# Optimization experiments

Measured on AMD Instinct MI355X. Metric: run time of the kernel, lower is better.

## Reference

```python
import jax, jax.numpy as jnp
import numpy as np

EMBED_DIM = 1024
NUM_HEADS = 16
HEAD_DIM = EMBED_DIM // NUM_HEADS


def setup_inputs() -> dict:
    key = jax.random.key(0)
    ks = jax.random.split(key, 11)
    B, S, D = 2, 2048, EMBED_DIM
    s = 1.0 / np.sqrt(D)
    inp = {
        "query": jax.random.normal(ks[0], (B, S, D), jnp.float32),
        "key": jax.random.normal(ks[1], (B, S, D), jnp.float32),
        "value": jax.random.normal(ks[2], (B, S, D), jnp.float32),
        # torch Linear weights: [out, in]
        "Wq": jax.random.normal(ks[3], (D, D), jnp.float32) * s,
        "bq": jnp.zeros((D,), jnp.float32),
        "Wk": jax.random.normal(ks[4], (D, D), jnp.float32) * s,
        "bk": jnp.zeros((D,), jnp.float32),
        "Wv": jax.random.normal(ks[5], (D, D), jnp.float32) * s,
        "bv": jnp.zeros((D,), jnp.float32),
        "Wo": jax.random.normal(ks[6], (D, D), jnp.float32) * s,
        "bo": jnp.zeros((D,), jnp.float32),
    }
    return inp


def reference(query, key, value, Wq, bq, Wk, bk, Wv, bv, Wo, bo):
    B, Q, D = query.shape
    K = key.shape[1]
    H, Hd = NUM_HEADS, HEAD_DIM
    # NOTE: source divides by scaling = head_dim**-0.5, i.e. multiplies by sqrt(head_dim)
    scaling = float(Hd) ** (-0.5)

    q = (query @ Wq.T + bq).reshape(B, Q, H, Hd).transpose(0, 2, 1, 3)  # [B,H,Q,Hd]
    k = (key @ Wk.T + bk).reshape(B, K, H, Hd).transpose(0, 2, 1, 3)    # [B,H,K,Hd]
    v = (value @ Wv.T + bv).reshape(B, K, H, Hd).transpose(0, 2, 1, 3)  # [B,H,K,Hd]

    scores = jnp.einsum("bhqd,bhkd->bhqk", q, k) / scaling
    attn = jax.nn.softmax(scores, axis=-1)  # dropout=0 (eval)
    out = jnp.einsum("bhqk,bhkd->bhqd", attn, v)
    out = out.transpose(0, 2, 1, 3).reshape(B, Q, D)
    return out @ Wo.T + bo
```

## Files before the change

kernel.cpp:

```cpp
#include <hip/hip_runtime.h>
#include <type_traits>
#include <utility>

#define B_ 2
#define S_ 2048
#define D_ 1024
#define H_ 16
#define HD_ 64
#define KDIM 1024

typedef __attribute__((ext_vector_type(8))) short    s16x8;
typedef __attribute__((ext_vector_type(8))) _Float16 h16x8;
typedef __attribute__((ext_vector_type(4))) float    f32x4;
typedef __attribute__((ext_vector_type(4))) int      i32x4;
typedef __attribute__((ext_vector_type(2))) int      i32x2;

template <typename T, typename = void> struct mfma_takes : std::false_type {};
template <typename T>
struct mfma_takes<T, std::void_t<decltype(__builtin_amdgcn_mfma_f32_16x16x32_f16(
    std::declval<T>(), std::declval<T>(), std::declval<f32x4>(), 0, 0, 0))>>
    : std::true_type {};
using frag8 = std::conditional_t<mfma_takes<h16x8>::value, h16x8, s16x8>;

__device__ __forceinline__ f32x4 mfma_f16(frag8 a, frag8 b, f32x4 c) {
  return __builtin_amdgcn_mfma_f32_16x16x32_f16(a, b, c, 0, 0, 0);
}

__device__ __forceinline__ short f2h(float f) {
  _Float16 h = (_Float16)f;
  short s; __builtin_memcpy(&s, &h, 2);
  return s;
}
__device__ __forceinline__ int pk2h(float a, float b) {
  auto p = __builtin_amdgcn_cvt_pkrtz(a, b);
  int r; __builtin_memcpy(&r, &p, 4); return r;
}
__device__ __forceinline__ frag8 ld_frag(const short* p) {
  return __builtin_bit_cast(frag8, *(const i32x4*)p);
}
__device__ __forceinline__ float fast_exp2(float x) {
  return __builtin_amdgcn_exp2f(x);
}

typedef __attribute__((address_space(1))) const void gvoid;
typedef __attribute__((address_space(3))) void lvoid;
__device__ __forceinline__ void async_copy16(const void* g, void* l) {
  __builtin_amdgcn_global_load_lds((gvoid*)g, (lvoid*)l, 16, 0, 0);
}

#define RAW_BARRIER() asm volatile("s_barrier" ::: "memory")
#define WAITCNT_VM(n) asm volatile("s_waitcnt vmcnt(" #n ")" ::: "memory")

__global__ __launch_bounds__(256)
void conv_all(const float* __restrict__ q, const float* __restrict__ k,
              const float* __restrict__ v, const float* __restrict__ Wq,
              const float* __restrict__ Wk, const float* __restrict__ Wv,
              const float* __restrict__ Wo,
              short* __restrict__ qh, short* __restrict__ kh,
              short* __restrict__ vh, short* __restrict__ wq,
              short* __restrict__ wk, short* __restrict__ wv,
              short* __restrict__ wo) {
  const int blk = blockIdx.x;
  const float* src; short* dst; int base;
  if (blk < 2048)      { src = q;  dst = qh; base = blk; }
  else if (blk < 4096) { src = k;  dst = kh; base = blk - 2048; }
  else if (blk < 6144) { src = v;  dst = vh; base = blk - 4096; }
  else if (blk < 6656) { src = Wq; dst = wq; base = blk - 6144; }
  else if (blk < 7168) { src = Wk; dst = wk; base = blk - 6656; }
  else if (blk < 7680) { src = Wv; dst = wv; base = blk - 7168; }
  else                 { src = Wo; dst = wo; base = blk - 7680; }
  const int i = base * 2048 + threadIdx.x * 8;
  float4 a0 = *(const float4*)(src + i);
  float4 a1 = *(const float4*)(src + i + 4);
  short h[8] = { f2h(a0.x), f2h(a0.y), f2h(a0.z), f2h(a0.w),
                 f2h(a1.x), f2h(a1.y), f2h(a1.z), f2h(a1.w) };
  i32x4 ph; __builtin_memcpy(&ph, h, 16);
  *(i32x4*)(dst + i) = ph;
}

__global__ __launch_bounds__(256, 3)
void gemm_qkv(const short* __restrict__ qh, const short* __restrict__ kh,
              const short* __restrict__ vh, const short* __restrict__ wq,
              const short* __restrict__ wk, const short* __restrict__ wv,
              const float* __restrict__ bq, const float* __restrict__ bk,
              const float* __restrict__ bv, short* __restrict__ Qf,
              short* __restrict__ Kf, short* __restrict__ Vt, float QS) {
  __shared__ short As[3 * 4096];
  __shared__ short Bs[3 * 4096];

  const int blk = blockIdx.x;
  const int xcd = blk & 7, i = blk >> 3;
  const int p = (i >> 3) * 8 + xcd;
  const int bn = i & 7;
  const int z = p >> 5, bm = p & 31;
  const short* Ap = z == 0 ? qh : z == 1 ? kh : vh;
  const short* Wp = z == 0 ? wq : z == 1 ? wk : wv;
  const float* bias = z == 0 ? bq : z == 1 ? bk : bv;
  short* Out = z == 0 ? Qf : z == 1 ? Kf : Vt;
  const float scale = z == 0 ? QS : 1.0f;
  const int omode = z == 2 ? 2 : 1;

  const int t = threadIdx.x, wave = t >> 6, lane = t & 63;
  const int laneN = lane & 15, quad = lane >> 4;
  const int wm = wave & 1, wn = wave >> 1;

  f32x4 acc[4][4];
#pragma unroll
  for (int i2 = 0; i2 < 4; ++i2)
#pragma unroll
    for (int j = 0; j < 4; ++j)
#pragma unroll
      for (int r = 0; r < 4; ++r) acc[i2][j][r] = 0.f;

  auto stage = [&](int buf, int kk) {
#pragma unroll
    for (int j = 0; j < 2; ++j) {
      const int chunk = j * 256 + t;
      const int row = chunk >> 2;
      const int gg = (chunk & 3) ^ ((row >> 1) & 3);
      async_copy16(Ap + (size_t)(bm * 128 + row) * KDIM + kk + gg * 8,
                   As + buf * 4096 + chunk * 8);
      async_copy16(Wp + (size_t)(bn * 128 + row) * KDIM + kk + gg * 8,
                   Bs + buf * 4096 + chunk * 8);
    }
  };

  stage(0, 0);
  stage(1, 32);
  int buf = 0;
  for (int kk = 0; kk < KDIM; kk += 32) {
    if (kk + 64 < KDIM) {
      int nb = buf + 2; if (nb >= 3) nb -= 3;
      stage(nb, kk + 64);
      WAITCNT_VM(8);
    } else if (kk + 32 < KDIM) {
      WAITCNT_VM(4);
    } else {
      WAITCNT_VM(0);
    }
    RAW_BARRIER();

    frag8 aF[4], bF[4];
#pragma unroll
    for (int mi = 0; mi < 4; ++mi) {
      const int row = wm * 64 + mi * 16 + laneN;
      aF[mi] = ld_frag(As + buf * 4096 + row * 32 +
                       ((quad ^ ((row >> 1) & 3)) * 8));
    }
#pragma unroll
    for (int ni = 0; ni < 4; ++ni) {
      const int row = wn * 64 + ni * 16 + laneN;
      bF[ni] = ld_frag(Bs + buf * 4096 + row * 32 +
                       ((quad ^ ((row >> 1) & 3)) * 8));
    }
#pragma unroll
    for (int mi = 0; mi < 4; ++mi)
#pragma unroll
      for (int ni = 0; ni < 4; ++ni)
        acc[mi][ni] = mfma_f16(aF[mi], bF[ni], acc[mi][ni]);
    RAW_BARRIER();
    buf = buf + 1 == 3 ? 0 : buf + 1;
  }

#pragma unroll
  for (int mi = 0; mi < 4; ++mi)
#pragma unroll
    for (int ni = 0; ni < 4; ++ni) {
      const int colg = bn * 128 + wn * 64 + ni * 16 + laneN;
      const float bb = bias[colg];
      if (omode == 2) {
        const int rowg0 = bm * 128 + wm * 64 + mi * 16 + quad * 4;
        const int b = rowg0 >> 11, s0 = rowg0 & 2047;
        const int h = colg >> 6, hd = colg & 63;
        short pk[4];
#pragma unroll
        for (int r = 0; r < 4; ++r) pk[r] = f2h(acc[mi][ni][r] + bb);
        i32x2 w; __builtin_memcpy(&w, pk, 8);
        *(i32x2*)(Vt + (((size_t)(b * H_ + h)) * HD_ + hd) * S_ + s0) = w;
      } else {
#pragma unroll
        for (int r = 0; r < 4; ++r) {
          const int rowg = bm * 128 + wm * 64 + mi * 16 + quad * 4 + r;
          const int b = rowg >> 11, s = rowg & 2047;
          const int h = colg >> 6, hd = colg & 63;
          Out[(((size_t)(b * H_ + h)) * S_ + s) * HD_ + hd] =
              f2h((acc[mi][ni][r] + bb) * scale);
        }
      }
    }
}

__global__ __launch_bounds__(256, 3)
void gemm_out(const short* __restrict__ Ap, const short* __restrict__ Wp,
              const float* __restrict__ bias, float* __restrict__ Out) {
  __shared__ short As[3 * 4096];
  __shared__ short Bs[3 * 2048];
  const int blk = blockIdx.x;
  const int xcd = blk & 7, i = blk >> 3;
  const int bm = (i >> 4) * 8 + xcd;
  const int bn = i & 15;

  const int t = threadIdx.x, wave = t >> 6, lane = t & 63;
  const int laneN = lane & 15, quad = lane >> 4;
  const int wm = wave & 1, wn = wave >> 1;

  f32x4 acc[4][2];
#pragma unroll
  for (int i2 = 0; i2 < 4; ++i2)
#pragma unroll
    for (int j = 0; j < 2; ++j)
#pragma unroll
      for (int r = 0; r < 4; ++r) acc[i2][j][r] = 0.f;

  auto stage = [&](int buf, int kk) {
#pragma unroll
    for (int j = 0; j < 2; ++j) {
      const int chunk = j * 256 + t;
      const int row = chunk >> 2;
      const int gg = (chunk & 3) ^ ((row >> 1) & 3);
      async_copy16(Ap + (size_t)(bm * 128 + row) * KDIM + kk + gg * 8,
                   As + buf * 4096 + chunk * 8);
    }
    {
      const int chunk = t;
      const int row = chunk >> 2;
      const int gg = (chunk & 3) ^ ((row >> 1) & 3);
      async_copy16(Wp + (size_t)(bn * 64 + row) * KDIM + kk + gg * 8,
                   Bs + buf * 2048 + chunk * 8);
    }
  };

  stage(0, 0);
  stage(1, 32);
  int buf = 0;
  for (int kk = 0; kk < KDIM; kk += 32) {
    if (kk + 64 < KDIM) {
      int nb = buf + 2; if (nb >= 3) nb -= 3;
      stage(nb, kk + 64);
      WAITCNT_VM(6);
    } else if (kk + 32 < KDIM) {
      WAITCNT_VM(3);
    } else {
      WAITCNT_VM(0);
    }
    RAW_BARRIER();

    frag8 aF[4], bF[2];
#pragma unroll
    for (int mi = 0; mi < 4; ++mi) {
      const int row = wm * 64 + mi * 16 + laneN;
      aF[mi] = ld_frag(As + buf * 4096 + row * 32 +
                       ((quad ^ ((row >> 1) & 3)) * 8));
    }
#pragma unroll
    for (int ni = 0; ni < 2; ++ni) {
      const int row = wn * 32 + ni * 16 + laneN;
      bF[ni] = ld_frag(Bs + buf * 2048 + row * 32 +
                       ((quad ^ ((row >> 1) & 3)) * 8));
    }
#pragma unroll
    for (int mi = 0; mi < 4; ++mi)
#pragma unroll
      for (int ni = 0; ni < 2; ++ni)
        acc[mi][ni] = mfma_f16(aF[mi], bF[ni], acc[mi][ni]);
    RAW_BARRIER();
    buf = buf + 1 == 3 ? 0 : buf + 1;
  }

#pragma unroll
  for (int mi = 0; mi < 4; ++mi)
#pragma unroll
    for (int ni = 0; ni < 2; ++ni) {
      const int colg = bn * 64 + wn * 32 + ni * 16 + laneN;
      const float bb = bias[colg];
#pragma unroll
      for (int r = 0; r < 4; ++r) {
        const int rowg = bm * 128 + wm * 64 + mi * 16 + quad * 4 + r;
        Out[(size_t)rowg * 1024 + colg] = acc[mi][ni][r] + bb;
      }
    }
}

__global__ __launch_bounds__(512, 2)
void attn(const short* __restrict__ Qf, const short* __restrict__ Kf,
          const short* __restrict__ Vt_, short* __restrict__ Ow) {
  __shared__ short Ks[2 * 4096];
  __shared__ short Vts[2 * 4096];
  __shared__ short Ps[8][16 * 72];

  const int blk = blockIdx.x;
  const int xcd = blk & 7, local = blk >> 3;
  const int pair = xcd * 4 + (local >> 4);
  const int h = pair & 15, b = pair >> 4, qt = local & 15;
  const size_t head = ((size_t)b * H_ + h) * (size_t)S_ * HD_;

  const int t = threadIdx.x;
  const int wave = t >> 6, lane = t & 63;
  const int laneN = lane & 15, quad = lane >> 4;

  frag8 qf[2];
  {
    const size_t row = (size_t)qt * 128 + wave * 16 + laneN;
#pragma unroll
    for (int half = 0; half < 2; ++half)
      qf[half] = ld_frag(Qf + head + row * HD_ + half * 32 + quad * 8);
  }

  f32x4 o[4];
  float m_r = -1e30f, l_r = 0.f;
#pragma unroll
  for (int i = 0; i < 4; ++i)
#pragma unroll
    for (int j = 0; j < 4; ++j) o[i][j] = 0.f;

  auto stage = [&](int buf, int kt) {
    const int chunk = t;
    const int row = chunk >> 3;
    const int g = (chunk & 7) ^ (row & 7);
    const int ldsoff = buf * 4096 + chunk * 8;
    async_copy16(Kf + head + (size_t)(kt * 64 + row) * HD_ + g * 8, Ks + ldsoff);
    async_copy16(Vt_ + head + (size_t)row * S_ + kt * 64 + g * 8, Vts + ldsoff);
  };

  stage(0, 0);
  int buf = 0;
  for (int kt = 0; kt < 32; ++kt, buf ^= 1) {
    if (kt + 1 < 32) {
      stage(buf ^ 1, kt + 1);
      WAITCNT_VM(2);
    } else {
      WAITCNT_VM(0);
    }
    RAW_BARRIER();

    frag8 vf[4][2];
#pragma unroll
    for (int dt = 0; dt < 4; ++dt) {
      const int row = dt * 16 + laneN;
#pragma unroll
      for (int half = 0; half < 2; ++half)
        vf[dt][half] = ld_frag(Vts + buf * 4096 + row * 64 +
                               (((half * 4 + quad) ^ (row & 7)) * 8));
    }

    f32x4 s[4];
#pragma unroll
    for (int nt = 0; nt < 4; ++nt) {
      const int row = nt * 16 + laneN;
      const int o0 = buf * 4096 + row * 64 + ((quad ^ (row & 7)) * 8);
      const int o1 = buf * 4096 + row * 64 + (((quad + 4) ^ (row & 7)) * 8);
      frag8 k0 = ld_frag(Ks + o0), k1 = ld_frag(Ks + o1);
      f32x4 acc;
#pragma unroll
      for (int j = 0; j < 4; ++j) acc[j] = 0.f;
      acc = mfma_f16(k0, qf[0], acc);
      acc = mfma_f16(k1, qf[1], acc);
      s[nt] = acc;
    }

    {
      float mx = -1e30f;
#pragma unroll
      for (int nt = 0; nt < 4; ++nt)
#pragma unroll
        for (int r = 0; r < 4; ++r) mx = fmaxf(mx, s[nt][r]);
      mx = fmaxf(mx, __shfl_xor(mx, 16));
      mx = fmaxf(mx, __shfl_xor(mx, 32));
      const float mold = m_r;
      const float mn = fmaxf(mold, mx);
      float rs = 0.f;
#pragma unroll
      for (int nt = 0; nt < 4; ++nt)
#pragma unroll
        for (int r = 0; r < 4; ++r) {
          const float p = fast_exp2(s[nt][r] - mn);
          s[nt][r] = p; rs += p;
        }
      rs += __shfl_xor(rs, 16);
      rs += __shfl_xor(rs, 32);
      if (__any(mn > mold)) {
        const float al = fast_exp2(mold - mn);
        m_r = mn;
        l_r = l_r * al + rs;
#pragma unroll
        for (int dt = 0; dt < 4; ++dt)
#pragma unroll
          for (int r = 0; r < 4; ++r) o[dt][r] *= al;
      } else {
        l_r += rs;
      }
    }

#pragma unroll
    for (int nt = 0; nt < 4; ++nt) {
      i32x2 w;
      w[0] = pk2h(s[nt][0], s[nt][1]);
      w[1] = pk2h(s[nt][2], s[nt][3]);
      *(i32x2*)&Ps[wave][laneN * 72 + nt * 16 + quad * 4] = w;
    }
    const frag8 p0 = ld_frag(&Ps[wave][laneN * 72 + quad * 8]);
    const frag8 p1 = ld_frag(&Ps[wave][laneN * 72 + 32 + quad * 8]);
#pragma unroll
    for (int dt = 0; dt < 4; ++dt) {
      o[dt] = mfma_f16(vf[dt][0], p0, o[dt]);
      o[dt] = mfma_f16(vf[dt][1], p1, o[dt]);
    }
    RAW_BARRIER();
  }

  {
    const float inv = 1.0f / l_r;
    const int sg = qt * 128 + wave * 16 + laneN;
    short* dst = Ow + ((size_t)b * S_ + sg) * D_ + h * HD_;
#pragma unroll
    for (int dt = 0; dt < 4; ++dt) {
      short pk[4] = { f2h(o[dt][0] * inv), f2h(o[dt][1] * inv),
                      f2h(o[dt][2] * inv), f2h(o[dt][3] * inv) };
      i32x2 w; __builtin_memcpy(&w, pk, 8);
      *(i32x2*)(dst + dt * 16 + quad * 4) = w;
    }
  }
}

extern "C" void kernel_launch(void* const* d_in, const int* in_sizes, int n_in,
                              void* d_out, int out_size, void* d_ws, size_t ws_size,
                              hipStream_t stream) {
  const float* q  = (const float*)d_in[0];
  const float* k  = (const float*)d_in[1];
  const float* v  = (const float*)d_in[2];
  const float* Wq = (const float*)d_in[3];
  const float* bq = (const float*)d_in[4];
  const float* Wk = (const float*)d_in[5];
  const float* bk = (const float*)d_in[6];
  const float* Wv = (const float*)d_in[7];
  const float* bv = (const float*)d_in[8];
  const float* Wo = (const float*)d_in[9];
  const float* bo = (const float*)d_in[10];

  const size_t NTOK = (size_t)B_ * S_ * D_;
  const size_t NW   = (size_t)D_ * D_;
  short* p = (short*)d_ws;
  short* qh = p; p += NTOK;  short* kh = p; p += NTOK;  short* vh = p; p += NTOK;
  short* wq = p; p += NW;    short* wk = p; p += NW;
  short* wv = p; p += NW;    short* wo = p; p += NW;
  short* Qf = p; p += NTOK;  short* Kf = p; p += NTOK;
  short* Vt = p; p += NTOK;  short* Ow = p; p += NTOK;

  dim3 blk(256);

  conv_all<<<8192, blk, 0, stream>>>(q, k, v, Wq, Wk, Wv, Wo,
                                     qh, kh, vh, wq, wk, wv, wo);

  const float QS = 11.541560327111707f;
  gemm_qkv<<<768, blk, 0, stream>>>(qh, kh, vh, wq, wk, wv, bq, bk, bv,
                                    Qf, Kf, Vt, QS);

  attn<<<512, dim3(512), 0, stream>>>(Qf, Kf, Vt, Ow);

  gemm_out<<<512, blk, 0, stream>>>(Ow, wo, bo, (float*)d_out);
}
```

Baseline: 225.3 us.

## Shrink attention blocks to 64 queries, swizzle P tile, lazy softmax rescale

The attention kernel now runs 256-thread blocks covering 64 query rows each, with twice as many blocks, and stages K/V with two async copies per thread. This gives finer scheduling granularity, but each block reloads the full K/V stream, so K/V traffic per query doubles. The P scratch tile drops its padding and uses an XOR/rotate swizzle to avoid LDS bank conflicts. Online softmax now rescales only when the row max grows by more than 8 in log2 units, skipping most rescale work while risking slightly larger exponent values.

```diff
diff --git a/kernel.cpp b/kernel.cpp
--- a/kernel.cpp
+++ b/kernel.cpp
@@ -281,17 +281,17 @@
     }
 }
 
-__global__ __launch_bounds__(512, 2)
+__global__ __launch_bounds__(256, 4)
 void attn(const short* __restrict__ Qf, const short* __restrict__ Kf,
           const short* __restrict__ Vt_, short* __restrict__ Ow) {
   __shared__ short Ks[2 * 4096];
   __shared__ short Vts[2 * 4096];
-  __shared__ short Ps[8][16 * 72];
+  __shared__ short Ps[4][16 * 64];
 
   const int blk = blockIdx.x;
   const int xcd = blk & 7, local = blk >> 3;
-  const int pair = xcd * 4 + (local >> 4);
-  const int h = pair & 15, b = pair >> 4, qt = local & 15;
+  const int pair = xcd * 4 + (local >> 5);
+  const int h = pair & 15, b = pair >> 4, qt = local & 31;
   const size_t head = ((size_t)b * H_ + h) * (size_t)S_ * HD_;
 
   const int t = threadIdx.x;
@@ -300,7 +300,7 @@
 
   frag8 qf[2];
   {
-    const size_t row = (size_t)qt * 128 + wave * 16 + laneN;
+    const size_t row = (size_t)qt * 64 + wave * 16 + laneN;
 #pragma unroll
     for (int half = 0; half < 2; ++half)
       qf[half] = ld_frag(Qf + head + row * HD_ + half * 32 + quad * 8);
@@ -314,32 +314,44 @@
     for (int j = 0; j < 4; ++j) o[i][j] = 0.f;
 
   auto stage = [&](int buf, int kt) {
-    const int chunk = t;
-    const int row = chunk >> 3;
-    const int g = (chunk & 7) ^ (row & 7);
-    const int ldsoff = buf * 4096 + chunk * 8;
-    async_copy16(Kf + head + (size_t)(kt * 64 + row) * HD_ + g * 8, Ks + ldsoff);
-    async_copy16(Vt_ + head + (size_t)row * S_ + kt * 64 + g * 8, Vts + ldsoff);
+#pragma unroll
+    for (int j = 0; j < 2; ++j) {
+      const int chunk = j * 256 + t;
+      const int row = chunk >> 3;
+      const int g = (chunk & 7) ^ (row & 7);
+      const int ldsoff = buf * 4096 + chunk * 8;
+      async_copy16(Kf + head + (size_t)(kt * 64 + row) * HD_ + g * 8,
+                   Ks + ldsoff);
+      async_copy16(Vt_ + head + (size_t)row * S_ + kt * 64 + g * 8,
+                   Vts + ldsoff);
+    }
   };
+
+  short* const pwr = &Ps[wave][0] + laneN * 64;
+  const int rd0 = ((quad + laneN) & 7) * 8;
+  const int rd1 = (((quad + 4) + laneN) & 7) * 8;
 
   stage(0, 0);
   int buf = 0;
   for (int kt = 0; kt < 32; ++kt, buf ^= 1) {
     if (kt + 1 < 32) {
       stage(buf ^ 1, kt + 1);
-      WAITCNT_VM(2);
+      WAITCNT_VM(4);
     } else {
       WAITCNT_VM(0);
     }
     RAW_BARRIER();
 
+    const short* Kb = Ks + buf * 4096;
+    const short* Vb = Vts + buf * 4096;
+
     frag8 vf[4][2];
 #pragma unroll
     for (int dt = 0; dt < 4; ++dt) {
       const int row = dt * 16 + laneN;
 #pragma unroll
       for (int half = 0; half < 2; ++half)
-        vf[dt][half] = ld_frag(Vts + buf * 4096 + row * 64 +
+        vf[dt][half] = ld_frag(Vb + row * 64 +
                                (((half * 4 + quad) ^ (row & 7)) * 8));
     }
 
@@ -347,9 +359,8 @@
 #pragma unroll
     for (int nt = 0; nt < 4; ++nt) {
       const int row = nt * 16 + laneN;
-      const int o0 = buf * 4096 + row * 64 + ((quad ^ (row & 7)) * 8);
-      const int o1 = buf * 4096 + row * 64 + (((quad + 4) ^ (row & 7)) * 8);
-      frag8 k0 = ld_frag(Ks + o0), k1 = ld_frag(Ks + o1);
+      frag8 k0 = ld_frag(Kb + row * 64 + ((quad ^ (row & 7)) * 8));
+      frag8 k1 = ld_frag(Kb + row * 64 + (((quad + 4) ^ (row & 7)) * 8));
       f32x4 acc;
 #pragma unroll
       for (int j = 0; j < 4; ++j) acc[j] = 0.f;
@@ -359,36 +370,37 @@
     }
 
     {
-      float mx = -1e30f;
+      float mt[4];
 #pragma unroll
       for (int nt = 0; nt < 4; ++nt)
-#pragma unroll
-        for (int r = 0; r < 4; ++r) mx = fmaxf(mx, s[nt][r]);
+        mt[nt] = fmaxf(fmaxf(s[nt][0], s[nt][1]), fmaxf(s[nt][2], s[nt][3]));
+      float mx = fmaxf(fmaxf(mt[0], mt[1]), fmaxf(mt[2], mt[3]));
       mx = fmaxf(mx, __shfl_xor(mx, 16));
       mx = fmaxf(mx, __shfl_xor(mx, 32));
-      const float mold = m_r;
-      const float mn = fmaxf(mold, mx);
-      float rs = 0.f;
-#pragma unroll
-      for (int nt = 0; nt < 4; ++nt)
-#pragma unroll
-        for (int r = 0; r < 4; ++r) {
-          const float p = fast_exp2(s[nt][r] - mn);
-          s[nt][r] = p; rs += p;
-        }
+      if (__any(mx > m_r + 8.f)) {
+        const float mn = fmaxf(m_r, mx);
+        const float al = fast_exp2(m_r - mn);
+        m_r = mn;
+        l_r *= al;
+#pragma unroll
+        for (int dt = 0; dt < 4; ++dt)
+#pragma unroll
+          for (int r = 0; r < 4; ++r) o[dt][r] *= al;
+      }
+      float rt[4];
+#pragma unroll
+      for (int nt = 0; nt < 4; ++nt) {
+        const float p0 = fast_exp2(s[nt][0] - m_r);
+        const float p1 = fast_exp2(s[nt][1] - m_r);
+        const float p2 = fast_exp2(s[nt][2] - m_r);
+        const float p3 = fast_exp2(s[nt][3] - m_r);
+        s[nt][0] = p0; s[nt][1] = p1; s[nt][2] = p2; s[nt][3] = p3;
+        rt[nt] = (p0 + p1) + (p2 + p3);
+      }
+      float rs = (rt[0] + rt[1]) + (rt[2] + rt[3]);
       rs += __shfl_xor(rs, 16);
       rs += __shfl_xor(rs, 32);
-      if (__any(mn > mold)) {
-        const float al = fast_exp2(mold - mn);
-        m_r = mn;
-        l_r = l_r * al + rs;
-#pragma unroll
-        for (int dt = 0; dt < 4; ++dt)
-#pragma unroll
-          for (int r = 0; r < 4; ++r) o[dt][r] *= al;
-      } else {
-        l_r += rs;
-      }
+      l_r += rs;
     }
 
 #pragma unroll
@@ -396,10 +408,12 @@
       i32x2 w;
       w[0] = pk2h(s[nt][0], s[nt][1]);
       w[1] = pk2h(s[nt][2], s[nt][3]);
-      *(i32x2*)&Ps[wave][laneN * 72 + nt * 16 + quad * 4] = w;
-    }
-    const frag8 p0 = ld_frag(&Ps[wave][laneN * 72 + quad * 8]);
-    const frag8 p1 = ld_frag(&Ps[wave][laneN * 72 + 32 + quad * 8]);
+      const int g = nt * 2 + (quad >> 1);
+      const int slot = (g + laneN) & 7;
+      *(i32x2*)(pwr + slot * 8 + (quad & 1) * 4) = w;
+    }
+    const frag8 p0 = ld_frag(pwr + rd0);
+    const frag8 p1 = ld_frag(pwr + rd1);
 #pragma unroll
     for (int dt = 0; dt < 4; ++dt) {
       o[dt] = mfma_f16(vf[dt][0], p0, o[dt]);
@@ -410,7 +424,7 @@
 
   {
     const float inv = 1.0f / l_r;
-    const int sg = qt * 128 + wave * 16 + laneN;
+    const int sg = qt * 64 + wave * 16 + laneN;
     short* dst = Ow + ((size_t)b * S_ + sg) * D_ + h * HD_;
 #pragma unroll
     for (int dt = 0; dt < 4; ++dt) {
@@ -455,7 +469,7 @@
   gemm_qkv<<<768, blk, 0, stream>>>(qh, kh, vh, wq, wk, wv, bq, bk, bv,
                                     Qf, Kf, Vt, QS);
 
-  attn<<<512, dim3(512), 0, stream>>>(Qf, Kf, Vt, Ow);
+  attn<<<1024, dim3(256), 0, stream>>>(Qf, Kf, Vt, Ow);
 
   gemm_out<<<512, blk, 0, stream>>>(Ow, wo, bo, (float*)d_out);
 }
```

Measured after the change: 233.2 us. 3.5% more time.
